# Performance work log

Measured on AMD Instinct MI355X. Metric: run time of the kernel, lower is better.

## Reference

```python
import jax, jax.numpy as jnp
import numpy as np

B, T, C, HEAD = 8, 2048, 1024, 64


def setup_inputs() -> dict:
    key = jax.random.key(0)
    kx, kq, kk, kv = jax.random.split(key, 4)
    x = jax.random.normal(kx, (B, T, C), dtype=jnp.float32)
    Wq = jax.random.normal(kq, (C, HEAD), dtype=jnp.float32) * (C ** -0.5)
    Wk = jax.random.normal(kk, (C, HEAD), dtype=jnp.float32) * (C ** -0.5)
    Wv = jax.random.normal(kv, (C, HEAD), dtype=jnp.float32) * (C ** -0.5)
    return {"x": x, "Wq": Wq, "Wk": Wk, "Wv": Wv}


def reference(x, Wq, Wk, Wv):
    # q,k,v: [B, T, H] via bias-free linear projections
    q = jnp.einsum('btc,ch->bth', x, Wq)
    k = jnp.einsum('btc,ch->bth', x, Wk)
    v = jnp.einsum('btc,ch->bth', x, Wv)
    scale = k.shape[-1] ** -0.5
    # scores: [B, T, T]
    scores = jnp.einsum('bqh,bkh->bqk', q, k) * scale
    Tq = x.shape[1]
    causal = jnp.tril(jnp.ones((Tq, Tq), dtype=bool))  # [T, T]
    scores = jnp.where(causal[None, :, :], scores, -jnp.inf)
    # softmax forced to fp32 in the original (autocast block)
    weight = jax.nn.softmax(scores.astype(jnp.float32), axis=-1)
    # dropout is identity in eval / p=0 deterministic baseline
    out = jnp.einsum('bqk,bkh->bqh', weight.astype(v.dtype), v)  # [B, T, H]
    return out
```

## Files before the change

### kernel.cpp

```cpp
#include <hip/hip_runtime.h>
#include <hip/hip_bf16.h>
#include <stdint.h>

#define NB 8
#define NT 2048
#define NC 1024
#define NH 64

typedef __attribute__((ext_vector_type(8))) short bf16x8;
typedef __attribute__((ext_vector_type(4))) float f32x4;

#define MFMA(a, b, c) __builtin_amdgcn_mfma_f32_16x16x32_bf16((a), (b), (c), 0, 0, 0)

static __device__ __forceinline__ short f2bf(float f) {
  union { float f; uint32_t u; } v; v.f = f;
  uint32_t r = v.u + 0x7FFFu + ((v.u >> 16) & 1u);
  return (short)(r >> 16);
}
static __device__ __forceinline__ float bf2f(short h) {
  union { uint32_t u; float f; } v; v.u = ((uint32_t)(uint16_t)h) << 16;
  return v.f;
}
static __device__ __forceinline__ void gload_lds16(const void* g, void* l) {
  __builtin_amdgcn_global_load_lds(
      (const __attribute__((address_space(1))) uint32_t*)g,
      (__attribute__((address_space(3))) uint32_t*)l, 16, 0, 0);
}

__global__ __launch_bounds__(256) void w_prep(const float* __restrict__ Wq,
                                              const float* __restrict__ Wk,
                                              const float* __restrict__ Wv,
                                              short* __restrict__ Wt) {
  __shared__ short tile[64][68];
  const int blk = blockIdx.x;
  const int mat = blk / 16;
  const int k0 = (blk % 16) * 64;
  const float* W = (mat == 0) ? Wq : (mat == 1) ? Wk : Wv;
  const float scale = (mat == 0) ? 0.125f * 1.44269504088896f : 1.0f;
  const int tid = threadIdx.x;
  {
    int kk = tid >> 2;
    int h0 = (tid & 3) * 16;
    const float* src = W + (size_t)(k0 + kk) * NH + h0;
#pragma unroll
    for (int i = 0; i < 16; ++i) tile[kk][h0 + i] = f2bf(src[i] * scale);
  }
  __syncthreads();
  {
    int j = tid >> 2;
    int kk0 = (tid & 3) * 16;
    bf16x8 t0, t1;
#pragma unroll
    for (int i = 0; i < 8; ++i) { t0[i] = tile[kk0 + i][j]; t1[i] = tile[kk0 + 8 + i][j]; }
    short* dst = Wt + (size_t)(mat * 64 + j) * NC + k0 + kk0;
    *(bf16x8*)dst = t0;
    *(bf16x8*)(dst + 8) = t1;
  }
}

__global__ __launch_bounds__(512) void qkv_proj(const float* __restrict__ x,
                                                const short* __restrict__ Wt,
                                                short* __restrict__ Qo,
                                                short* __restrict__ Ko,
                                                short* __restrict__ VTo) {
  __shared__ char lds_raw[2][32768];
  const int tid = threadIdx.x;
  const int lane = tid & 63;
  const int wave = tid >> 6;
  const int l15 = lane & 15;
  const int hi = lane >> 4;
  const int m0 = blockIdx.x * 32;
  const int wr = wave & 1;
  const int wc = wave >> 1;

  f32x4 acc[3];
#pragma unroll
  for (int f = 0; f < 3; ++f) acc[f] = (f32x4){0.f, 0.f, 0.f, 0.f};

  int xr, xc;
  {
    int off = tid * 16;
    int ol = off ^ (((off >> 8) & 7) << 4);
    xr = ol >> 8; xc = (ol >> 2) & 63;
  }
  int wrow[3], wcol[3];
#pragma unroll
  for (int i = 0; i < 3; ++i) {
    int off = i * 8192 + tid * 16;
    int ol = off ^ (((off >> 7) & 7) << 4);
    wrow[i] = ol >> 7; wcol[i] = (ol >> 1) & 63;
  }

#define STAGE(k0, buf)                                                          \
  {                                                                             \
    char* xsb_ = lds_raw[buf];                                                  \
    char* wtb_ = lds_raw[buf] + 8192;                                           \
    gload_lds16(x + (size_t)(m0 + xr) * NC + (k0) + xc, xsb_ + tid * 16);       \
    _Pragma("unroll")                                                           \
    for (int i = 0; i < 3; ++i)                                                 \
      gload_lds16(Wt + (size_t)wrow[i] * NC + (k0) + wcol[i],                   \
                  wtb_ + i * 8192 + tid * 16);                                  \
  }

  STAGE(0, 0);
  __syncthreads();
  int cur = 0;
  for (int t = 0; t < 16; ++t) {
    if (t + 1 < 16) STAGE((t + 1) * 64, cur ^ 1);
    const char* xsb = lds_raw[cur];
    const char* wtb = lds_raw[cur] + 8192;
    const int r = wr * 16 + l15;
#pragma unroll
    for (int s = 0; s < 2; ++s) {
      int o1 = (r * 256 + s * 128 + hi * 32) ^ ((r & 7) << 4);
      int o2 = (r * 256 + s * 128 + hi * 32 + 16) ^ ((r & 7) << 4);
      float4 q0 = *(const float4*)(xsb + o1);
      float4 q1 = *(const float4*)(xsb + o2);
      bf16x8 a;
      a[0] = f2bf(q0.x); a[1] = f2bf(q0.y); a[2] = f2bf(q0.z); a[3] = f2bf(q0.w);
      a[4] = f2bf(q1.x); a[5] = f2bf(q1.y); a[6] = f2bf(q1.z); a[7] = f2bf(q1.w);
#pragma unroll
      for (int f = 0; f < 3; ++f) {
        int c = wc * 48 + f * 16 + l15;
        int ob = (c * 128 + s * 64 + hi * 16) ^ ((c & 7) << 4);
        bf16x8 b = *(const bf16x8*)(wtb + ob);
        acc[f] = MFMA(a, b, acc[f]);
      }
    }
    __syncthreads();
    cur ^= 1;
  }
#undef STAGE

#pragma unroll
  for (int f = 0; f < 3; ++f) {
    int c = wc * 48 + f * 16 + l15;
    int mat = c >> 6, h = c & 63;
    if (mat < 2) {
      short* dst = (mat == 0) ? Qo : Ko;
#pragma unroll
      for (int r = 0; r < 4; ++r) {
        int t = m0 + wr * 16 + hi * 4 + r;
        dst[(size_t)t * NH + h] = f2bf(acc[f][r]);
      }
    } else {
      int bb = m0 >> 11;
      int t0 = (m0 & 2047) + wr * 16 + hi * 4;
      short4 v;
      v.x = f2bf(acc[f][0]); v.y = f2bf(acc[f][1]);
      v.z = f2bf(acc[f][2]); v.w = f2bf(acc[f][3]);
      *(short4*)(VTo + ((size_t)(bb * 64 + h)) * NT + t0) = v;
    }
  }
}

__global__ __launch_bounds__(256, 2) void attn_fused(const short* __restrict__ Q,
                                                     const short* __restrict__ K,
                                                     const short* __restrict__ Vt,
                                                     float* __restrict__ out) {
  __shared__ short PO[4][32][72];
  __shared__ float Ls[4][32];

  const int tid = threadIdx.x;
  const int lane = tid & 63;
  const int wave = tid >> 6;
  const int l15 = lane & 15;
  const int hi = lane >> 4;
  const int kg = hi * 8;

  const int bid = blockIdx.x;
  const int half = bid >> 8;
  const int rr = bid & 255;
  const int b = rr >> 5;
  const int i = rr & 31;
  const int qt = (half == 0) ? (63 - i) : i;
  const int ktmax = qt >> 1;
  const int q0 = qt * 32;

  bf16x8 qf[2][2];
#pragma unroll
  for (int m = 0; m < 2; ++m)
#pragma unroll
    for (int s = 0; s < 2; ++s)
      qf[m][s] = *(const bf16x8*)(Q + ((size_t)b * NT + q0 + m * 16 + l15) * NH +
                                  s * 32 + kg);

  f32x4 oacc[2][4];
#pragma unroll
  for (int m = 0; m < 2; ++m)
#pragma unroll
    for (int f = 0; f < 4; ++f) oacc[m][f] = (f32x4){0.f, 0.f, 0.f, 0.f};
  float ps[2][4];
#pragma unroll
  for (int m = 0; m < 2; ++m)
#pragma unroll
    for (int r = 0; r < 4; ++r) ps[m][r] = 0.f;

#define LOAD_K(dst, kt_)                                                        \
  {                                                                             \
    const short* kb_ = K + ((size_t)b * NT + (kt_) * 64) * NH;                  \
    _Pragma("unroll") for (int n = 0; n < 4; ++n)                               \
    _Pragma("unroll") for (int s = 0; s < 2; ++s)                               \
      dst[n][s] = *(const bf16x8*)(kb_ + (n * 16 + l15) * NH + s * 32 + kg);    \
  }
#define LOAD_V(dst, kt_)                                                        \
  {                                                                             \
    _Pragma("unroll") for (int f = 0; f < 4; ++f)                               \
    _Pragma("unroll") for (int s = 0; s < 2; ++s)                               \
      dst[f][s] = *(const bf16x8*)(Vt + ((size_t)(b * 64 + f * 16 + l15)) * NT +\
                                   (kt_) * 64 + s * 32 + kg);                   \
  }

  int kt = wave;
  bf16x8 kf[4][2];
  if (kt <= ktmax) LOAD_K(kf, kt);

  for (; kt <= ktmax; kt += 4) {
    bf16x8 vf[4][2];
    LOAD_V(vf, kt);

    f32x4 S[2][4];
#pragma unroll
    for (int m = 0; m < 2; ++m)
#pragma unroll
      for (int n = 0; n < 4; ++n) {
        S[m][n] = (f32x4){0.f, 0.f, 0.f, 0.f};
        S[m][n] = MFMA(qf[m][0], kf[n][0], S[m][n]);
        S[m][n] = MFMA(qf[m][1], kf[n][1], S[m][n]);
      }

    bf16x8 kn[4][2];
    const bool more = (kt + 4) <= ktmax;
    if (more) LOAD_K(kn, kt + 4);

    if (kt == ktmax) {
#pragma unroll
      for (int m = 0; m < 2; ++m)
#pragma unroll
        for (int n = 0; n < 4; ++n)
#pragma unroll
          for (int r = 0; r < 4; ++r)
            if (kt * 64 + n * 16 + l15 > q0 + m * 16 + hi * 4 + r)
              S[m][n][r] = -INFINITY;
    }
#pragma unroll
    for (int m = 0; m < 2; ++m)
#pragma unroll
      for (int n = 0; n < 4; ++n)
#pragma unroll
        for (int r = 0; r < 4; ++r) {
          float p = __builtin_amdgcn_exp2f(S[m][n][r]);
          S[m][n][r] = p;
          ps[m][r] += p;
        }

#pragma unroll
    for (int m = 0; m < 2; ++m)
#pragma unroll
      for (int n = 0; n < 4; ++n)
#pragma unroll
        for (int r = 0; r < 4; ++r)
          PO[wave][m * 16 + hi * 4 + r][n * 16 + l15] = f2bf(S[m][n][r]);

    bf16x8 pa[2][2];
#pragma unroll
    for (int m = 0; m < 2; ++m)
#pragma unroll
      for (int s = 0; s < 2; ++s)
        pa[m][s] = *(const bf16x8*)&PO[wave][m * 16 + l15][s * 32 + kg];
#pragma unroll
    for (int m = 0; m < 2; ++m)
#pragma unroll
      for (int f = 0; f < 4; ++f) {
        oacc[m][f] = MFMA(pa[m][0], vf[f][0], oacc[m][f]);
        oacc[m][f] = MFMA(pa[m][1], vf[f][1], oacc[m][f]);
      }
    if (more) {
#pragma unroll
      for (int n = 0; n < 4; ++n)
#pragma unroll
        for (int s = 0; s < 2; ++s) kf[n][s] = kn[n][s];
    }
  }
#undef LOAD_K
#undef LOAD_V

#pragma unroll
  for (int d = 1; d < 16; d <<= 1)
#pragma unroll
    for (int m = 0; m < 2; ++m)
#pragma unroll
      for (int r = 0; r < 4; ++r) ps[m][r] += __shfl_xor(ps[m][r], d);

  if (l15 == 0) {
#pragma unroll
    for (int m = 0; m < 2; ++m)
#pragma unroll
      for (int r = 0; r < 4; ++r)
        Ls[wave][m * 16 + hi * 4 + r] = ps[m][r];
  }
#pragma unroll
  for (int m = 0; m < 2; ++m)
#pragma unroll
    for (int f = 0; f < 4; ++f)
#pragma unroll
      for (int r = 0; r < 4; ++r)
        PO[wave][m * 16 + hi * 4 + r][f * 16 + l15] = f2bf(oacc[m][f][r]);
  __syncthreads();

  {
    const int row = tid >> 3;
    const int c0 = (tid & 7) * 8;
    float L = 0.f;
    float o[8] = {0.f, 0.f, 0.f, 0.f, 0.f, 0.f, 0.f, 0.f};
#pragma unroll
    for (int w = 0; w < 4; ++w) {
      L += Ls[w][row];
      short4 v0 = *(const short4*)&PO[w][row][c0];
      short4 v1 = *(const short4*)&PO[w][row][c0 + 4];
      o[0] += bf2f(v0.x); o[1] += bf2f(v0.y); o[2] += bf2f(v0.z); o[3] += bf2f(v0.w);
      o[4] += bf2f(v1.x); o[5] += bf2f(v1.y); o[6] += bf2f(v1.z); o[7] += bf2f(v1.w);
    }
    float inv = 1.f / L;
    float* po = out + ((size_t)b * NT + q0 + row) * NH + c0;
    float4 r0 = {o[0] * inv, o[1] * inv, o[2] * inv, o[3] * inv};
    float4 r1 = {o[4] * inv, o[5] * inv, o[6] * inv, o[7] * inv};
    *(float4*)po = r0;
    *(float4*)(po + 4) = r1;
  }
}

extern "C" void kernel_launch(void* const* d_in, const int* in_sizes, int n_in,
                              void* d_out, int out_size, void* d_ws, size_t ws_size,
                              hipStream_t stream) {
  const float* x  = (const float*)d_in[0];
  const float* Wq = (const float*)d_in[1];
  const float* Wk = (const float*)d_in[2];
  const float* Wv = (const float*)d_in[3];
  float* out = (float*)d_out;

  char* ws = (char*)d_ws;
  short* Wt = (short*)ws;
  short* Qb = (short*)(ws + (size_t)(1 << 20));
  short* Kb = (short*)(ws + (size_t)(3 << 20));
  short* Vt = (short*)(ws + (size_t)(5 << 20));

  hipLaunchKernelGGL(w_prep, dim3(48), dim3(256), 0, stream, Wq, Wk, Wv, Wt);
  hipLaunchKernelGGL(qkv_proj, dim3(512), dim3(512), 0, stream, x, Wt, Qb, Kb, Vt);
  hipLaunchKernelGGL(attn_fused, dim3(512), dim3(256), 0, stream, Qb, Kb, Vt, out);
}
```

Measured before the change: 48.00 us.

## Load projection weights directly into registers and shrink QKV block to 4 waves

The QKV projection kernel no longer stages the transposed weights through LDS. Each wave reads its 48 weight columns straight from global memory into registers every k-step. Block size drops from 512 to 256 threads, with each wave now covering both 16-row slabs of x, so each weight fragment is reused across two MFMAs. The aim is to cut LDS traffic and footprint (16KB instead of 64KB) and raise occupancy, at the cost of uncached-by-LDS global weight loads on the critical path each iteration.

```diff
diff --git a/kernel.cpp b/kernel.cpp
--- a/kernel.cpp
+++ b/kernel.cpp
@@ -58,48 +58,48 @@
   }
 }
 
-__global__ __launch_bounds__(512) void qkv_proj(const float* __restrict__ x,
-                                                const short* __restrict__ Wt,
-                                                short* __restrict__ Qo,
-                                                short* __restrict__ Ko,
-                                                short* __restrict__ VTo) {
-  __shared__ char lds_raw[2][32768];
+__global__ __launch_bounds__(256, 4) void qkv_proj(const float* __restrict__ x,
+                                                   const short* __restrict__ Wt,
+                                                   short* __restrict__ Qo,
+                                                   short* __restrict__ Ko,
+                                                   short* __restrict__ VTo) {
+  __shared__ char xbuf[2][8192];
   const int tid = threadIdx.x;
   const int lane = tid & 63;
   const int wave = tid >> 6;
   const int l15 = lane & 15;
   const int hi = lane >> 4;
   const int m0 = blockIdx.x * 32;
-  const int wr = wave & 1;
-  const int wc = wave >> 1;
-
-  f32x4 acc[3];
-#pragma unroll
-  for (int f = 0; f < 3; ++f) acc[f] = (f32x4){0.f, 0.f, 0.f, 0.f};
-
-  int xr, xc;
-  {
-    int off = tid * 16;
+
+  f32x4 acc[2][3];
+#pragma unroll
+  for (int m = 0; m < 2; ++m)
+#pragma unroll
+    for (int f = 0; f < 3; ++f) acc[m][f] = (f32x4){0.f, 0.f, 0.f, 0.f};
+
+  int xr[2], xc[2];
+#pragma unroll
+  for (int i = 0; i < 2; ++i) {
+    int off = i * 4096 + tid * 16;
     int ol = off ^ (((off >> 8) & 7) << 4);
-    xr = ol >> 8; xc = (ol >> 2) & 63;
-  }
-  int wrow[3], wcol[3];
-#pragma unroll
-  for (int i = 0; i < 3; ++i) {
-    int off = i * 8192 + tid * 16;
-    int ol = off ^ (((off >> 7) & 7) << 4);
-    wrow[i] = ol >> 7; wcol[i] = (ol >> 1) & 63;
+    xr[i] = ol >> 8; xc[i] = (ol >> 2) & 63;
+  }
+
+  const short* wsrc[6];
+#pragma unroll
+  for (int f = 0; f < 3; ++f) {
+    int c = wave * 48 + f * 16 + l15;
+#pragma unroll
+    for (int s = 0; s < 2; ++s)
+      wsrc[f * 2 + s] = Wt + (size_t)c * NC + s * 32 + hi * 8;
   }
 
 #define STAGE(k0, buf)                                                          \
   {                                                                             \
-    char* xsb_ = lds_raw[buf];                                                  \
-    char* wtb_ = lds_raw[buf] + 8192;                                           \
-    gload_lds16(x + (size_t)(m0 + xr) * NC + (k0) + xc, xsb_ + tid * 16);       \
     _Pragma("unroll")                                                           \
-    for (int i = 0; i < 3; ++i)                                                 \
-      gload_lds16(Wt + (size_t)wrow[i] * NC + (k0) + wcol[i],                   \
-                  wtb_ + i * 8192 + tid * 16);                                  \
+    for (int i = 0; i < 2; ++i)                                                 \
+      gload_lds16(x + (size_t)(m0 + xr[i]) * NC + (k0) + xc[i],                 \
+                  &xbuf[buf][i * 4096 + tid * 16]);                             \
   }
 
   STAGE(0, 0);
@@ -107,25 +107,28 @@
   int cur = 0;
   for (int t = 0; t < 16; ++t) {
     if (t + 1 < 16) STAGE((t + 1) * 64, cur ^ 1);
-    const char* xsb = lds_raw[cur];
-    const char* wtb = lds_raw[cur] + 8192;
-    const int r = wr * 16 + l15;
+    bf16x8 wt[6];
+#pragma unroll
+    for (int i = 0; i < 6; ++i) wt[i] = *(const bf16x8*)(wsrc[i] + (size_t)t * 64);
+    const char* xsb = xbuf[cur];
 #pragma unroll
     for (int s = 0; s < 2; ++s) {
-      int o1 = (r * 256 + s * 128 + hi * 32) ^ ((r & 7) << 4);
-      int o2 = (r * 256 + s * 128 + hi * 32 + 16) ^ ((r & 7) << 4);
-      float4 q0 = *(const float4*)(xsb + o1);
-      float4 q1 = *(const float4*)(xsb + o2);
-      bf16x8 a;
-      a[0] = f2bf(q0.x); a[1] = f2bf(q0.y); a[2] = f2bf(q0.z); a[3] = f2bf(q0.w);
-      a[4] = f2bf(q1.x); a[5] = f2bf(q1.y); a[6] = f2bf(q1.z); a[7] = f2bf(q1.w);
-#pragma unroll
-      for (int f = 0; f < 3; ++f) {
-        int c = wc * 48 + f * 16 + l15;
-        int ob = (c * 128 + s * 64 + hi * 16) ^ ((c & 7) << 4);
-        bf16x8 b = *(const bf16x8*)(wtb + ob);
-        acc[f] = MFMA(a, b, acc[f]);
+      bf16x8 a[2];
+#pragma unroll
+      for (int m = 0; m < 2; ++m) {
+        int r = m * 16 + l15;
+        int o1 = (r * 256 + s * 128 + hi * 32) ^ ((r & 7) << 4);
+        int o2 = (r * 256 + s * 128 + hi * 32 + 16) ^ ((r & 7) << 4);
+        float4 q0 = *(const float4*)(xsb + o1);
+        float4 q1 = *(const float4*)(xsb + o2);
+        a[m][0] = f2bf(q0.x); a[m][1] = f2bf(q0.y); a[m][2] = f2bf(q0.z); a[m][3] = f2bf(q0.w);
+        a[m][4] = f2bf(q1.x); a[m][5] = f2bf(q1.y); a[m][6] = f2bf(q1.z); a[m][7] = f2bf(q1.w);
       }
+#pragma unroll
+      for (int m = 0; m < 2; ++m)
+#pragma unroll
+        for (int f = 0; f < 3; ++f)
+          acc[m][f] = MFMA(a[m], wt[f * 2 + s], acc[m][f]);
     }
     __syncthreads();
     cur ^= 1;
@@ -134,22 +137,25 @@
 
 #pragma unroll
   for (int f = 0; f < 3; ++f) {
-    int c = wc * 48 + f * 16 + l15;
+    int c = wave * 48 + f * 16 + l15;
     int mat = c >> 6, h = c & 63;
-    if (mat < 2) {
-      short* dst = (mat == 0) ? Qo : Ko;
-#pragma unroll
-      for (int r = 0; r < 4; ++r) {
-        int t = m0 + wr * 16 + hi * 4 + r;
-        dst[(size_t)t * NH + h] = f2bf(acc[f][r]);
+#pragma unroll
+    for (int m = 0; m < 2; ++m) {
+      if (mat < 2) {
+        short* dst = (mat == 0) ? Qo : Ko;
+#pragma unroll
+        for (int r = 0; r < 4; ++r) {
+          int t = m0 + m * 16 + hi * 4 + r;
+          dst[(size_t)t * NH + h] = f2bf(acc[m][f][r]);
+        }
+      } else {
+        int bb = m0 >> 11;
+        int t0 = (m0 & 2047) + m * 16 + hi * 4;
+        short4 v;
+        v.x = f2bf(acc[m][f][0]); v.y = f2bf(acc[m][f][1]);
+        v.z = f2bf(acc[m][f][2]); v.w = f2bf(acc[m][f][3]);
+        *(short4*)(VTo + ((size_t)(bb * 64 + h)) * NT + t0) = v;
       }
-    } else {
-      int bb = m0 >> 11;
-      int t0 = (m0 & 2047) + wr * 16 + hi * 4;
-      short4 v;
-      v.x = f2bf(acc[f][0]); v.y = f2bf(acc[f][1]);
-      v.z = f2bf(acc[f][2]); v.w = f2bf(acc[f][3]);
-      *(short4*)(VTo + ((size_t)(bb * 64 + h)) * NT + t0) = v;
     }
   }
 }
@@ -346,6 +352,6 @@
   short* Vt = (short*)(ws + (size_t)(5 << 20));
 
   hipLaunchKernelGGL(w_prep, dim3(48), dim3(256), 0, stream, Wq, Wk, Wv, Wt);
-  hipLaunchKernelGGL(qkv_proj, dim3(512), dim3(512), 0, stream, x, Wt, Qb, Kb, Vt);
+  hipLaunchKernelGGL(qkv_proj, dim3(512), dim3(256), 0, stream, x, Wt, Qb, Kb, Vt);
   hipLaunchKernelGGL(attn_fused, dim3(512), dim3(256), 0, stream, Qb, Kb, Vt, out);
 }
```

New measurement: 58.70 us. 1.22x slower.

## Deepen QKV projection pipeline with 4-stage x prefetch and fewer waves

Applied to the files above, without the earlier changes.

The QKV projection kernel now runs 256 threads per block instead of 512, and each wave computes 6 output fragments instead of 3. The x tile now goes through a 4-deep LDS ring prefetched three steps ahead, with weights double-buffered. Explicit vmcnt waits and a single barrier per iteration replace the old two-sync double buffer. The aim is to hide global-load latency for x, which is the dominant memory stream, and to cut synchronisation overhead. The cost is more registers per thread and hand-tuned vmcnt counts that must match the issue order exactly.

```diff
diff --git a/kernel.cpp b/kernel.cpp
--- a/kernel.cpp
+++ b/kernel.cpp
@@ -58,94 +58,107 @@
   }
 }
 
-__global__ __launch_bounds__(512) void qkv_proj(const float* __restrict__ x,
+__global__ __launch_bounds__(256) void qkv_proj(const float* __restrict__ x,
                                                 const short* __restrict__ Wt,
                                                 short* __restrict__ Qo,
                                                 short* __restrict__ Ko,
                                                 short* __restrict__ VTo) {
-  __shared__ char lds_raw[2][32768];
+  __shared__ char xbuf[4][8192];
+  __shared__ char wbuf[2][24576];
   const int tid = threadIdx.x;
   const int lane = tid & 63;
   const int wave = tid >> 6;
   const int l15 = lane & 15;
   const int hi = lane >> 4;
   const int m0 = blockIdx.x * 32;
-  const int wr = wave & 1;
-  const int wc = wave >> 1;
-
-  f32x4 acc[3];
-#pragma unroll
-  for (int f = 0; f < 3; ++f) acc[f] = (f32x4){0.f, 0.f, 0.f, 0.f};
-
-  int xr, xc;
-  {
-    int off = tid * 16;
+  const int mr = (wave & 1) * 16;
+  const int ncol = (wave >> 1) * 96;
+
+  f32x4 acc[6];
+#pragma unroll
+  for (int f = 0; f < 6; ++f) acc[f] = (f32x4){0.f, 0.f, 0.f, 0.f};
+
+  int xr[2], xc[2];
+#pragma unroll
+  for (int i = 0; i < 2; ++i) {
+    int off = i * 4096 + tid * 16;
     int ol = off ^ (((off >> 8) & 7) << 4);
-    xr = ol >> 8; xc = (ol >> 2) & 63;
-  }
-  int wrow[3], wcol[3];
-#pragma unroll
-  for (int i = 0; i < 3; ++i) {
-    int off = i * 8192 + tid * 16;
+    xr[i] = ol >> 8; xc[i] = (ol & 255) >> 2;
+  }
+  int wrow[6], wcol[6];
+#pragma unroll
+  for (int i = 0; i < 6; ++i) {
+    int off = i * 4096 + tid * 16;
     int ol = off ^ (((off >> 7) & 7) << 4);
-    wrow[i] = ol >> 7; wcol[i] = (ol >> 1) & 63;
-  }
-
-#define STAGE(k0, buf)                                                          \
-  {                                                                             \
-    char* xsb_ = lds_raw[buf];                                                  \
-    char* wtb_ = lds_raw[buf] + 8192;                                           \
-    gload_lds16(x + (size_t)(m0 + xr) * NC + (k0) + xc, xsb_ + tid * 16);       \
-    _Pragma("unroll")                                                           \
-    for (int i = 0; i < 3; ++i)                                                 \
-      gload_lds16(Wt + (size_t)wrow[i] * NC + (k0) + wcol[i],                   \
-                  wtb_ + i * 8192 + tid * 16);                                  \
-  }
-
-  STAGE(0, 0);
-  __syncthreads();
-  int cur = 0;
+    wrow[i] = ol >> 7; wcol[i] = (ol & 127) >> 1;
+  }
+
+#define ISSUE_X(t)                                                              \
+  { _Pragma("unroll")                                                           \
+    for (int i = 0; i < 2; ++i)                                                 \
+      gload_lds16(x + (size_t)(m0 + xr[i]) * NC + (t) * 64 + xc[i],             \
+                  &xbuf[(t) & 3][i * 4096 + tid * 16]); }
+#define ISSUE_W(t)                                                              \
+  { _Pragma("unroll")                                                           \
+    for (int i = 0; i < 6; ++i)                                                 \
+      gload_lds16(Wt + (size_t)wrow[i] * NC + (t) * 64 + wcol[i],               \
+                  &wbuf[(t) & 1][i * 4096 + tid * 16]); }
+
+  ISSUE_X(0);
+  ISSUE_W(0);
+  ISSUE_X(1);
+  ISSUE_X(2);
+
+#pragma unroll
   for (int t = 0; t < 16; ++t) {
-    if (t + 1 < 16) STAGE((t + 1) * 64, cur ^ 1);
-    const char* xsb = lds_raw[cur];
-    const char* wtb = lds_raw[cur] + 8192;
-    const int r = wr * 16 + l15;
-#pragma unroll
-    for (int s = 0; s < 2; ++s) {
-      int o1 = (r * 256 + s * 128 + hi * 32) ^ ((r & 7) << 4);
-      int o2 = (r * 256 + s * 128 + hi * 32 + 16) ^ ((r & 7) << 4);
-      float4 q0 = *(const float4*)(xsb + o1);
-      float4 q1 = *(const float4*)(xsb + o2);
-      bf16x8 a;
-      a[0] = f2bf(q0.x); a[1] = f2bf(q0.y); a[2] = f2bf(q0.z); a[3] = f2bf(q0.w);
-      a[4] = f2bf(q1.x); a[5] = f2bf(q1.y); a[6] = f2bf(q1.z); a[7] = f2bf(q1.w);
-#pragma unroll
-      for (int f = 0; f < 3; ++f) {
-        int c = wc * 48 + f * 16 + l15;
-        int ob = (c * 128 + s * 64 + hi * 16) ^ ((c & 7) << 4);
-        bf16x8 b = *(const bf16x8*)(wtb + ob);
-        acc[f] = MFMA(a, b, acc[f]);
+    if (t == 0)       asm volatile("s_waitcnt vmcnt(4)" ::: "memory");
+    else if (t < 14)  asm volatile("s_waitcnt vmcnt(2)" ::: "memory");
+    else              asm volatile("s_waitcnt vmcnt(0)" ::: "memory");
+    __builtin_amdgcn_sched_barrier(0);
+    __builtin_amdgcn_s_barrier();
+    __builtin_amdgcn_sched_barrier(0);
+    if (t + 1 < 16) ISSUE_W(t + 1);
+    if (t + 3 < 16) ISSUE_X(t + 3);
+    {
+      const char* xsb = xbuf[t & 3];
+      const char* wtb = wbuf[t & 1];
+      const int r = mr + l15;
+#pragma unroll
+      for (int s = 0; s < 2; ++s) {
+        int o1 = (r * 256 + s * 128 + hi * 32) ^ ((r & 7) << 4);
+        int o2 = (r * 256 + s * 128 + hi * 32 + 16) ^ ((r & 7) << 4);
+        float4 q0 = *(const float4*)(xsb + o1);
+        float4 q1 = *(const float4*)(xsb + o2);
+        bf16x8 a;
+        a[0] = f2bf(q0.x); a[1] = f2bf(q0.y); a[2] = f2bf(q0.z); a[3] = f2bf(q0.w);
+        a[4] = f2bf(q1.x); a[5] = f2bf(q1.y); a[6] = f2bf(q1.z); a[7] = f2bf(q1.w);
+#pragma unroll
+        for (int f = 0; f < 6; ++f) {
+          int c = ncol + f * 16 + l15;
+          int ob = (c * 128 + s * 64 + hi * 16) ^ ((c & 7) << 4);
+          bf16x8 b = *(const bf16x8*)(wtb + ob);
+          acc[f] = MFMA(a, b, acc[f]);
+        }
       }
     }
-    __syncthreads();
-    cur ^= 1;
-  }
-#undef STAGE
-
-#pragma unroll
-  for (int f = 0; f < 3; ++f) {
-    int c = wc * 48 + f * 16 + l15;
-    int mat = c >> 6, h = c & 63;
+  }
+#undef ISSUE_X
+#undef ISSUE_W
+
+#pragma unroll
+  for (int f = 0; f < 6; ++f) {
+    int g = ncol + f * 16 + l15;
+    int mat = g >> 6, h = g & 63;
     if (mat < 2) {
       short* dst = (mat == 0) ? Qo : Ko;
 #pragma unroll
       for (int r = 0; r < 4; ++r) {
-        int t = m0 + wr * 16 + hi * 4 + r;
+        int t = m0 + mr + hi * 4 + r;
         dst[(size_t)t * NH + h] = f2bf(acc[f][r]);
       }
     } else {
       int bb = m0 >> 11;
-      int t0 = (m0 & 2047) + wr * 16 + hi * 4;
+      int t0 = (m0 & 2047) + mr + hi * 4;
       short4 v;
       v.x = f2bf(acc[f][0]); v.y = f2bf(acc[f][1]);
       v.z = f2bf(acc[f][2]); v.w = f2bf(acc[f][3]);
@@ -346,6 +359,6 @@
   short* Vt = (short*)(ws + (size_t)(5 << 20));
 
   hipLaunchKernelGGL(w_prep, dim3(48), dim3(256), 0, stream, Wq, Wk, Wv, Wt);
-  hipLaunchKernelGGL(qkv_proj, dim3(512), dim3(512), 0, stream, x, Wt, Qb, Kb, Vt);
+  hipLaunchKernelGGL(qkv_proj, dim3(512), dim3(256), 0, stream, x, Wt, Qb, Kb, Vt);
   hipLaunchKernelGGL(attn_fused, dim3(512), dim3(256), 0, stream, Qb, Kb, Vt, out);
 }
```

Result: slower. 49.01 us (+2.1%).

## Load projection weights directly into registers and shrink LDS to x-only double buffer

Applied to the files above, without the earlier changes.

The QKV projection kernel stops staging the transposed weight tile through LDS. Each wave now loads its B-fragments straight from global memory (L2-resident Wt) into registers every k-step, and only the x tile is double-buffered in LDS. This cuts LDS use from 64KB to 16KB, which together with launch_bounds(512,2) allows two blocks per CU and drops the LDS reads for weights. The cost is more global/L2 traffic per wave, since waves sharing columns reload the same weights, and the global loads now sit on the critical path before the MFMAs.

```diff
diff --git a/kernel.cpp b/kernel.cpp
--- a/kernel.cpp
+++ b/kernel.cpp
@@ -58,12 +58,12 @@
   }
 }
 
-__global__ __launch_bounds__(512) void qkv_proj(const float* __restrict__ x,
-                                                const short* __restrict__ Wt,
-                                                short* __restrict__ Qo,
-                                                short* __restrict__ Ko,
-                                                short* __restrict__ VTo) {
-  __shared__ char lds_raw[2][32768];
+__global__ __launch_bounds__(512, 2) void qkv_proj(const float* __restrict__ x,
+                                                   const short* __restrict__ Wt,
+                                                   short* __restrict__ Qo,
+                                                   short* __restrict__ Ko,
+                                                   short* __restrict__ VTo) {
+  __shared__ char xbuf[2][8192];
   const int tid = threadIdx.x;
   const int lane = tid & 63;
   const int wave = tid >> 6;
@@ -83,32 +83,28 @@
     int ol = off ^ (((off >> 8) & 7) << 4);
     xr = ol >> 8; xc = (ol >> 2) & 63;
   }
-  int wrow[3], wcol[3];
-#pragma unroll
-  for (int i = 0; i < 3; ++i) {
-    int off = i * 8192 + tid * 16;
-    int ol = off ^ (((off >> 7) & 7) << 4);
-    wrow[i] = ol >> 7; wcol[i] = (ol >> 1) & 63;
-  }
-
-#define STAGE(k0, buf)                                                          \
-  {                                                                             \
-    char* xsb_ = lds_raw[buf];                                                  \
-    char* wtb_ = lds_raw[buf] + 8192;                                           \
-    gload_lds16(x + (size_t)(m0 + xr) * NC + (k0) + xc, xsb_ + tid * 16);       \
-    _Pragma("unroll")                                                           \
-    for (int i = 0; i < 3; ++i)                                                 \
-      gload_lds16(Wt + (size_t)wrow[i] * NC + (k0) + wcol[i],                   \
-                  wtb_ + i * 8192 + tid * 16);                                  \
-  }
-
-  STAGE(0, 0);
+  const float* xsrc = x + (size_t)(m0 + xr) * NC + xc;
+
+  const short* wsrc[6];
+#pragma unroll
+  for (int f = 0; f < 3; ++f) {
+    int c = wc * 48 + f * 16 + l15;
+#pragma unroll
+    for (int s = 0; s < 2; ++s)
+      wsrc[f * 2 + s] = Wt + (size_t)c * NC + s * 32 + hi * 8;
+  }
+
+#define STAGEX(t) gload_lds16(xsrc + (size_t)(t) * 64, &xbuf[(t) & 1][tid * 16])
+
+  STAGEX(0);
   __syncthreads();
-  int cur = 0;
+#pragma unroll
   for (int t = 0; t < 16; ++t) {
-    if (t + 1 < 16) STAGE((t + 1) * 64, cur ^ 1);
-    const char* xsb = lds_raw[cur];
-    const char* wtb = lds_raw[cur] + 8192;
+    bf16x8 wt[6];
+#pragma unroll
+    for (int i = 0; i < 6; ++i) wt[i] = *(const bf16x8*)(wsrc[i] + (size_t)t * 64);
+    if (t + 1 < 16) STAGEX(t + 1);
+    const char* xsb = xbuf[t & 1];
     const int r = wr * 16 + l15;
 #pragma unroll
     for (int s = 0; s < 2; ++s) {
@@ -120,17 +116,12 @@
       a[0] = f2bf(q0.x); a[1] = f2bf(q0.y); a[2] = f2bf(q0.z); a[3] = f2bf(q0.w);
       a[4] = f2bf(q1.x); a[5] = f2bf(q1.y); a[6] = f2bf(q1.z); a[7] = f2bf(q1.w);
 #pragma unroll
-      for (int f = 0; f < 3; ++f) {
-        int c = wc * 48 + f * 16 + l15;
-        int ob = (c * 128 + s * 64 + hi * 16) ^ ((c & 7) << 4);
-        bf16x8 b = *(const bf16x8*)(wtb + ob);
-        acc[f] = MFMA(a, b, acc[f]);
-      }
+      for (int f = 0; f < 3; ++f)
+        acc[f] = MFMA(a, wt[f * 2 + s], acc[f]);
     }
     __syncthreads();
-    cur ^= 1;
-  }
-#undef STAGE
+  }
+#undef STAGEX
 
 #pragma unroll
   for (int f = 0; f < 3; ++f) {
```

Measured after the change: 76.85 us. 1.6x slower.
